# Performance work log

Hardware: AMD Instinct MI355X
Metric: run time of the kernel (lower is better)

The kernel has to match this reference:

```python
import jax, jax.numpy as jnp
import numpy as np

B, N_ATOMS, N_PROBES, N_EDGES = 4, 1250, 50000, 125000
T, D, SH_DIM, NUM_BASIS = 3, 128, 16, 10
CUTOFF = 4.0
NUM_NEIGHBORS = 20.0


def spherical_harmonics_l3(u):
    """Real spherical harmonics l=0..3, component normalization (||Y_l||^2 = 2l+1 on unit vectors). u: [E,3] unit vectors."""
    x, y, z = u[:, 0], u[:, 1], u[:, 2]
    x2, y2, z2 = x * x, y * y, z * z
    s3 = np.sqrt(3.0)
    s15 = np.sqrt(15.0)
    sh = [
        jnp.ones_like(x),                       # l=0
        s3 * x, s3 * y, s3 * z,                 # l=1
        s15 * x * y,                            # l=2
        s15 * y * z,
        (np.sqrt(5.0) / 2.0) * (3.0 * z2 - 1.0),
        s15 * x * z,
        (s15 / 2.0) * (x2 - y2),
        np.sqrt(35.0 / 8.0) * y * (3.0 * x2 - y2),   # l=3
        np.sqrt(105.0) * x * y * z,
        np.sqrt(21.0 / 8.0) * y * (5.0 * z2 - 1.0),
        (np.sqrt(7.0) / 2.0) * (5.0 * z2 * z - 3.0 * z),
        np.sqrt(21.0 / 8.0) * x * (5.0 * z2 - 1.0),
        (np.sqrt(105.0) / 2.0) * z * (x2 - y2),
        np.sqrt(35.0 / 8.0) * x * (x2 - 3.0 * y2),
    ]
    return jnp.stack(sh, axis=-1)  # [E, 16]


def radial_basis(r):
    """Normalized gaussian radial basis on [0, CUTOFF] (e3nn soft_one_hot_linspace style). r: [E]."""
    centers = jnp.linspace(0.0, CUTOFF, NUM_BASIS)
    step = CUTOFF / (NUM_BASIS - 1)
    diff = (r[:, None] - centers) / step
    return jnp.exp(-diff * diff) * 1.12  # [E, NUM_BASIS]


def setup_inputs() -> dict:
    key = jax.random.key(0)
    ks = jax.random.split(key, 10)
    atom_xyz = 6.0 * jax.random.uniform(ks[0], (B, N_ATOMS, 3), jnp.float32)
    probe_xyz = 6.0 * jax.random.uniform(ks[1], (B, N_PROBES, 3), jnp.float32)
    src = jax.random.randint(ks[2], (B, N_EDGES, 1), 0, N_ATOMS)
    dst = jax.random.randint(ks[3], (B, N_EDGES, 1), 0, N_PROBES)
    probe_edges = jnp.concatenate([src, dst], axis=-1).astype(jnp.int32)
    ped = jax.random.randint(ks[4], (B, N_EDGES, 3), -1, 2).astype(jnp.float32)
    cell = jnp.broadcast_to(6.0 * jnp.eye(3, dtype=jnp.float32), (B, 3, 3)) \
        + 0.05 * jax.random.normal(ks[5], (B, 3, 3), jnp.float32)
    atom_rep = jax.random.normal(ks[6], (T, B * N_ATOMS, D), jnp.float32)
    w1 = 0.3 * jax.random.normal(ks[7], (T, NUM_BASIS, 100), jnp.float32)
    w2 = 0.1 * jax.random.normal(ks[8], (T, 100, SH_DIM), jnp.float32)
    w_out = 0.05 * jax.random.normal(ks[9], (D, 1), jnp.float32)
    return {
        "atom_xyz": atom_xyz, "probe_xyz": probe_xyz, "probe_edges": probe_edges,
        "probe_edges_displacement": ped, "cell": cell,
        "num_nodes": jnp.full((B,), N_ATOMS, jnp.int32),
        "num_probes": jnp.full((B,), N_PROBES, jnp.int32),
        "num_probe_edges": jnp.full((B,), N_EDGES, jnp.int32),
        "atom_rep": atom_rep, "w1": w1, "w2": w2, "w_out": w_out,
    }


def reference(atom_xyz, probe_xyz, probe_edges, probe_edges_displacement, cell,
              num_nodes, num_probes, num_probe_edges, atom_rep, w1, w2, w_out):
    b, n = atom_xyz.shape[:2]
    p = probe_xyz.shape[1]
    atoms = atom_xyz.reshape(-1, 3)          # [b*n, 3]  (unpad_and_cat, equal lengths)
    probes_xyz = probe_xyz.reshape(-1, 3)    # [b*p, 3]
    zero = jnp.zeros((1,), num_nodes.dtype)
    node_off = jnp.cumsum(jnp.concatenate([zero, num_nodes[:-1]]))
    probe_off = jnp.cumsum(jnp.concatenate([zero, num_probes[:-1]]))
    off = jnp.stack([node_off, probe_off], axis=-1)[:, None, :]  # [b,1,2]
    edges = (probe_edges + off).reshape(-1, 2)                   # [E,2]
    src, dst = edges[:, 0], edges[:, 1]
    # fractional shift -> cartesian displacement via per-sample cell (repeat_interleave)
    disp = jnp.einsum('bec,bcd->bed', probe_edges_displacement, cell).reshape(-1, 3)
    vec = probes_xyz[dst] - (atoms[src] + disp)                  # [E,3]
    r = jnp.linalg.norm(vec, axis=1)
    u = vec / jnp.maximum(r, 1e-9)[:, None]
    sh = spherical_harmonics_l3(u)                               # [E,16]
    rb = radial_basis(r)                                         # [E,10]
    P = probes_xyz.shape[0]
    probes = jnp.zeros((P, atom_rep.shape[-1]), atom_xyz.dtype)
    inv_sqrt_nn = 1.0 / np.sqrt(NUM_NEIGHBORS)
    for t in range(atom_rep.shape[0]):  # small fixed number of interaction layers
        h = jax.nn.silu(rb @ w1[t]) @ w2[t]          # radial MLP -> per-edge sh weights [E,16]
        scal = jnp.sum(h * sh, axis=-1)              # contract with edge attr [E]
        msg = atom_rep[t][src] * scal[:, None]       # gather + modulate [E,D]
        probes = probes + jax.ops.segment_sum(msg, dst, num_segments=P) * inv_sqrt_nn
    out = (probes @ w_out)[:, 0].reshape(b, p)       # readout 0e scalar, pad_and_stack
    return out, probes
```

## Files before the change

kernel.cpp:

```cpp
#include <hip/hip_runtime.h>
#include <math.h>

#define B_ 4
#define NA 1250
#define NP 50000
#define NE 125000
#define T_ 3
#define D_ 128
#define SHD 16
#define NB 10
#define HID 100
#define E_TOT (B_*NE)
#define P_TOT (B_*NP)
#define A_TOT (B_*NA)
#define INV_SQRT_NN 0.22360679774997896f
#define SCAN_NBLK ((P_TOT + 1023) / 1024)

#define GRID_N 8192
#define RMAX 24.0f
#define FSTR (T_*SHD)

__global__ __launch_bounds__(256) void build_table_kernel(
    const float* __restrict__ w1, const float* __restrict__ w2,
    float* __restrict__ ftab)
{
    int idx = blockIdx.x*256 + threadIdx.x;
    if (idx >= T_*GRID_N) return;
    int t = idx >> 13;
    int ri = idx & (GRID_N-1);

    float r = (float)ri * (RMAX / (float)(GRID_N-1));
    float rb[NB];
    float rs = r * (9.0f / 4.0f);
    #pragma unroll
    for (int i = 0; i < NB; ++i) {
        float dif = rs - (float)i;
        rb[i] = __expf(-dif*dif) * 1.12f;
    }

    float fk[SHD];
    #pragma unroll
    for (int k = 0; k < SHD; ++k) fk[k] = 0.0f;

    for (int j = 0; j < HID; ++j) {
        float h = 0.0f;
        #pragma unroll
        for (int i = 0; i < NB; ++i)
            h += rb[i] * w1[(size_t)(t*NB + i)*HID + j];
        float s = h / (1.0f + __expf(-h));
        #pragma unroll
        for (int k = 0; k < SHD; ++k)
            fk[k] += s * w2[(size_t)(t*HID + j)*SHD + k];
    }

    float* dstp = ftab + (size_t)ri*FSTR + t*SHD;
    #pragma unroll
    for (int k = 0; k < SHD; ++k) dstp[k] = fk[k];
}

__global__ __launch_bounds__(256) void edge_kernel(
    const float* __restrict__ atom_xyz, const float* __restrict__ probe_xyz,
    const int* __restrict__ probe_edges, const float* __restrict__ ped,
    const float* __restrict__ cell, const float* __restrict__ ftab,
    int* __restrict__ counts, int* __restrict__ rank,
    int* __restrict__ dstf, int* __restrict__ srcf, float* __restrict__ scal)
{
    int e = blockIdx.x * 256 + threadIdx.x;
    if (e >= E_TOT) return;
    int b  = e / NE;
    int le = e - b * NE;

    int sl = probe_edges[(size_t)b*NE*2 + (size_t)le*2 + 0];
    int dl = probe_edges[(size_t)b*NE*2 + (size_t)le*2 + 1];
    int src = sl + b * NA;
    int dst = dl + b * NP;

    float p0 = ped[(size_t)b*NE*3 + (size_t)le*3 + 0];
    float p1 = ped[(size_t)b*NE*3 + (size_t)le*3 + 1];
    float p2 = ped[(size_t)b*NE*3 + (size_t)le*3 + 2];
    const float* cb = cell + b*9;
    float dx = p0*cb[0] + p1*cb[3] + p2*cb[6];
    float dy = p0*cb[1] + p1*cb[4] + p2*cb[7];
    float dz = p0*cb[2] + p1*cb[5] + p2*cb[8];

    float vx = probe_xyz[(size_t)dst*3+0] - (atom_xyz[(size_t)src*3+0] + dx);
    float vy = probe_xyz[(size_t)dst*3+1] - (atom_xyz[(size_t)src*3+1] + dy);
    float vz = probe_xyz[(size_t)dst*3+2] - (atom_xyz[(size_t)src*3+2] + dz);
    float r = sqrtf(vx*vx + vy*vy + vz*vz);
    float rinv = 1.0f / fmaxf(r, 1e-9f);
    float x = vx*rinv, y = vy*rinv, z = vz*rinv;
    float x2 = x*x, y2 = y*y, z2 = z*z;

    const float S3  = 1.7320508075688772f;
    const float S15 = 3.872983346207417f;
    float sh[SHD];
    sh[0]  = 1.0f;
    sh[1]  = S3 * x;
    sh[2]  = S3 * y;
    sh[3]  = S3 * z;
    sh[4]  = S15 * x * y;
    sh[5]  = S15 * y * z;
    sh[6]  = 1.118033988749895f * (3.0f*z2 - 1.0f);
    sh[7]  = S15 * x * z;
    sh[8]  = 1.9364916731037085f * (x2 - y2);
    sh[9]  = 2.091650066335189f  * y * (3.0f*x2 - y2);
    sh[10] = 10.246950765959598f * x * y * z;
    sh[11] = 1.6201851746019651f * y * (5.0f*z2 - 1.0f);
    sh[12] = 1.3228756555322954f * (5.0f*z2*z - 3.0f*z);
    sh[13] = 1.6201851746019651f * x * (5.0f*z2 - 1.0f);
    sh[14] = 5.123475382979799f  * z * (x2 - y2);
    sh[15] = 2.091650066335189f  * x * (x2 - 3.0f*y2);

    float u = r * ((float)(GRID_N-1) / RMAX);
    int i0 = (int)u;
    i0 = (i0 > GRID_N-2) ? (GRID_N-2) : i0;
    float w = u - (float)i0;
    const float* F0 = ftab + (size_t)i0 * FSTR;
    const float* F1 = F0 + FSTR;

    #pragma unroll
    for (int t = 0; t < T_; ++t) {
        float d0 = 0.0f, d1 = 0.0f;
        #pragma unroll
        for (int k = 0; k < SHD; ++k) {
            d0 += F0[t*SHD + k] * sh[k];
            d1 += F1[t*SHD + k] * sh[k];
        }
        scal[(size_t)e*3 + t] = d0 + w * (d1 - d0);
    }

    int rk = atomicAdd(&counts[dst], 1);
    rank[e] = rk;
    dstf[e] = dst;
    srcf[e] = src;
}

__global__ __launch_bounds__(256) void scan1_kernel(const int* __restrict__ counts,
                                                    int* __restrict__ starts,
                                                    int* __restrict__ bsums)
{
    __shared__ int sd[256];
    int base = blockIdx.x*1024 + threadIdx.x*4;
    int v0 = (base+0 < P_TOT) ? counts[base+0] : 0;
    int v1 = (base+1 < P_TOT) ? counts[base+1] : 0;
    int v2 = (base+2 < P_TOT) ? counts[base+2] : 0;
    int v3 = (base+3 < P_TOT) ? counts[base+3] : 0;
    int s = v0+v1+v2+v3;
    sd[threadIdx.x] = s;
    __syncthreads();
    for (int off = 1; off < 256; off <<= 1) {
        int t = (threadIdx.x >= off) ? sd[threadIdx.x - off] : 0;
        __syncthreads();
        sd[threadIdx.x] += t;
        __syncthreads();
    }
    int excl = sd[threadIdx.x] - s;
    if (base+0 < P_TOT) starts[base+0] = excl;
    if (base+1 < P_TOT) starts[base+1] = excl + v0;
    if (base+2 < P_TOT) starts[base+2] = excl + v0 + v1;
    if (base+3 < P_TOT) starts[base+3] = excl + v0 + v1 + v2;
    if (threadIdx.x == 255) bsums[blockIdx.x] = sd[255];
}

__global__ __launch_bounds__(256) void scan2_kernel(int* __restrict__ bsums, int n)
{
    __shared__ int sd[256];
    int s = (threadIdx.x < n) ? bsums[threadIdx.x] : 0;
    sd[threadIdx.x] = s;
    __syncthreads();
    for (int off = 1; off < 256; off <<= 1) {
        int t = (threadIdx.x >= off) ? sd[threadIdx.x - off] : 0;
        __syncthreads();
        sd[threadIdx.x] += t;
        __syncthreads();
    }
    if (threadIdx.x < n) bsums[threadIdx.x] = sd[threadIdx.x] - s;
}

__global__ __launch_bounds__(256) void scan3_kernel(int* __restrict__ starts,
                                                    const int* __restrict__ bsums)
{
    int add = bsums[blockIdx.x];
    int base = blockIdx.x*1024 + threadIdx.x*4;
    #pragma unroll
    for (int k = 0; k < 4; ++k)
        if (base+k < P_TOT) starts[base+k] += add;
}

__global__ __launch_bounds__(256) void scatter_kernel(const int* __restrict__ dstf,
                                                      const int* __restrict__ rank,
                                                      const int* __restrict__ starts,
                                                      const int* __restrict__ srcf,
                                                      const float* __restrict__ scal,
                                                      int* __restrict__ srcf_s,
                                                      float* __restrict__ scal_s)
{
    int e = blockIdx.x*256 + threadIdx.x;
    if (e >= E_TOT) return;
    int pos = starts[dstf[e]] + rank[e];
    srcf_s[pos] = srcf[e];
    float s0 = scal[(size_t)e*3+0];
    float s1 = scal[(size_t)e*3+1];
    float s2 = scal[(size_t)e*3+2];
    scal_s[(size_t)pos*3+0] = s0;
    scal_s[(size_t)pos*3+1] = s1;
    scal_s[(size_t)pos*3+2] = s2;
}

__global__ __launch_bounds__(256) void gather_kernel(
    const int* __restrict__ counts, const int* __restrict__ starts,
    const int* __restrict__ srcf_s, const float* __restrict__ scal_s,
    const float* __restrict__ atom_rep, const float* __restrict__ w_out,
    float* __restrict__ out, float* __restrict__ probes)
{
    int wave = threadIdx.x >> 6;
    int lane = threadIdx.x & 63;
    int p = blockIdx.x*4 + wave;

    int st  = starts[p];
    int cnt = counts[p];
    const float2* rep2 = (const float2*)atom_rep;
    const size_t TSTRIDE = (size_t)A_TOT * (D_/2);

    float ax = 0.0f, ay = 0.0f;
    for (int i = 0; i < cnt; ++i) {
        int src = srcf_s[st + i];
        float s0 = scal_s[(size_t)(st+i)*3 + 0];
        float s1 = scal_s[(size_t)(st+i)*3 + 1];
        float s2 = scal_s[(size_t)(st+i)*3 + 2];
        size_t ro = (size_t)src * (D_/2) + lane;
        float2 a0 = rep2[ro];
        float2 a1 = rep2[TSTRIDE + ro];
        float2 a2 = rep2[2*TSTRIDE + ro];
        ax += s0*a0.x + s1*a1.x + s2*a2.x;
        ay += s0*a0.y + s1*a1.y + s2*a2.y;
    }
    ax *= INV_SQRT_NN;
    ay *= INV_SQRT_NN;
    ((float2*)probes)[(size_t)p*(D_/2) + lane] = make_float2(ax, ay);

    float ov = ax*w_out[2*lane] + ay*w_out[2*lane+1];
    #pragma unroll
    for (int off = 32; off > 0; off >>= 1) ov += __shfl_down(ov, off);
    if (lane == 0) out[p] = ov;
}

extern "C" void kernel_launch(void* const* d_in, const int* in_sizes, int n_in,
                              void* d_out, int out_size, void* d_ws, size_t ws_size,
                              hipStream_t stream) {
    const float* atom_xyz  = (const float*)d_in[0];
    const float* probe_xyz = (const float*)d_in[1];
    const int*   probe_edges = (const int*)d_in[2];
    const float* ped       = (const float*)d_in[3];
    const float* cell      = (const float*)d_in[4];
    const float* atom_rep  = (const float*)d_in[8];
    const float* w1        = (const float*)d_in[9];
    const float* w2        = (const float*)d_in[10];
    const float* w_out     = (const float*)d_in[11];

    float* out    = (float*)d_out;
    float* probes = out + P_TOT;

    int* counts     = (int*)d_ws;
    int* starts     = counts + P_TOT;
    int* bsums      = starts + P_TOT;
    int* rank       = bsums + 256;
    int* dstf       = rank + E_TOT;
    int* srcf       = dstf + E_TOT;
    int* srcf_s     = srcf + E_TOT;
    float* scal     = (float*)(srcf_s + E_TOT);
    float* scal_s   = scal + (size_t)E_TOT*3;
    float* ftab     = scal_s + (size_t)E_TOT*3;

    hipMemsetAsync(counts, 0, P_TOT*sizeof(int), stream);

    build_table_kernel<<<(T_*GRID_N + 255)/256, 256, 0, stream>>>(w1, w2, ftab);

    edge_kernel<<<(E_TOT + 255)/256, 256, 0, stream>>>(
        atom_xyz, probe_xyz, probe_edges, ped, cell, ftab,
        counts, rank, dstf, srcf, scal);

    scan1_kernel<<<SCAN_NBLK, 256, 0, stream>>>(counts, starts, bsums);
    scan2_kernel<<<1, 256, 0, stream>>>(bsums, SCAN_NBLK);
    scan3_kernel<<<SCAN_NBLK, 256, 0, stream>>>(starts, bsums);
    scatter_kernel<<<(E_TOT + 255)/256, 256, 0, stream>>>(
        dstf, rank, starts, srcf, scal, srcf_s, scal_s);

    gather_kernel<<<P_TOT/4, 256, 0, stream>>>(
        counts, starts, srcf_s, scal_s, atom_rep, w_out, out, probes);
}
```

Before: 325.0 us.

## Count edges first, then fuse edge compute with CSR scatter into packed float4

A lightweight count pass now builds per-probe counts, the scan runs on them, and the edge kernel computes the scalars and writes them directly into their sorted slot as a packed float4 (three scalars plus the source index). This removes the separate scatter kernel and the intermediate rank, dst, src and scal arrays. The gather kernel reads one float4 per edge, unrolls by 4 so row loads overlap, uses readfirstlane for the segment bounds, and writes probes with nontemporal stores. The cost is a second atomic counter array and an extra pass that reads the edge list.

```diff
diff --git a/kernel.cpp b/kernel.cpp
--- a/kernel.cpp
+++ b/kernel.cpp
@@ -20,6 +20,8 @@
 #define RMAX 24.0f
 #define FSTR (T_*SHD)
 
+typedef float f32x2 __attribute__((ext_vector_type(2)));
+
 __global__ __launch_bounds__(256) void build_table_kernel(
     const float* __restrict__ w1, const float* __restrict__ w2,
     float* __restrict__ ftab)
@@ -58,26 +60,87 @@
     for (int k = 0; k < SHD; ++k) dstp[k] = fk[k];
 }
 
-__global__ __launch_bounds__(256) void edge_kernel(
+__global__ __launch_bounds__(256) void count_kernel(const int* __restrict__ probe_edges,
+                                                    int* __restrict__ counts)
+{
+    int e = blockIdx.x*256 + threadIdx.x;
+    if (e >= E_TOT) return;
+    int b = e / NE;
+    int dl = probe_edges[(size_t)e*2 + 1];
+    atomicAdd(&counts[dl + b*NP], 1);
+}
+
+__global__ __launch_bounds__(256) void scan1_kernel(const int* __restrict__ counts,
+                                                    int* __restrict__ starts,
+                                                    int* __restrict__ bsums)
+{
+    __shared__ int sd[256];
+    int base = blockIdx.x*1024 + threadIdx.x*4;
+    int v0 = (base+0 < P_TOT) ? counts[base+0] : 0;
+    int v1 = (base+1 < P_TOT) ? counts[base+1] : 0;
+    int v2 = (base+2 < P_TOT) ? counts[base+2] : 0;
+    int v3 = (base+3 < P_TOT) ? counts[base+3] : 0;
+    int s = v0+v1+v2+v3;
+    sd[threadIdx.x] = s;
+    __syncthreads();
+    for (int off = 1; off < 256; off <<= 1) {
+        int t = (threadIdx.x >= off) ? sd[threadIdx.x - off] : 0;
+        __syncthreads();
+        sd[threadIdx.x] += t;
+        __syncthreads();
+    }
+    int excl = sd[threadIdx.x] - s;
+    if (base+0 < P_TOT) starts[base+0] = excl;
+    if (base+1 < P_TOT) starts[base+1] = excl + v0;
+    if (base+2 < P_TOT) starts[base+2] = excl + v0 + v1;
+    if (base+3 < P_TOT) starts[base+3] = excl + v0 + v1 + v2;
+    if (threadIdx.x == 255) bsums[blockIdx.x] = sd[255];
+}
+
+__global__ __launch_bounds__(256) void scan2_kernel(int* __restrict__ bsums, int n)
+{
+    __shared__ int sd[256];
+    int s = (threadIdx.x < n) ? bsums[threadIdx.x] : 0;
+    sd[threadIdx.x] = s;
+    __syncthreads();
+    for (int off = 1; off < 256; off <<= 1) {
+        int t = (threadIdx.x >= off) ? sd[threadIdx.x - off] : 0;
+        __syncthreads();
+        sd[threadIdx.x] += t;
+        __syncthreads();
+    }
+    if (threadIdx.x < n) bsums[threadIdx.x] = sd[threadIdx.x] - s;
+}
+
+__global__ __launch_bounds__(256) void scan3_kernel(int* __restrict__ starts,
+                                                    const int* __restrict__ bsums)
+{
+    int add = bsums[blockIdx.x];
+    int base = blockIdx.x*1024 + threadIdx.x*4;
+    #pragma unroll
+    for (int k = 0; k < 4; ++k)
+        if (base+k < P_TOT) starts[base+k] += add;
+}
+
+__global__ __launch_bounds__(256) void edge_scatter_kernel(
     const float* __restrict__ atom_xyz, const float* __restrict__ probe_xyz,
     const int* __restrict__ probe_edges, const float* __restrict__ ped,
     const float* __restrict__ cell, const float* __restrict__ ftab,
-    int* __restrict__ counts, int* __restrict__ rank,
-    int* __restrict__ dstf, int* __restrict__ srcf, float* __restrict__ scal)
+    const int* __restrict__ starts, int* __restrict__ counts2,
+    float4* __restrict__ edge4)
 {
     int e = blockIdx.x * 256 + threadIdx.x;
     if (e >= E_TOT) return;
     int b  = e / NE;
-    int le = e - b * NE;
-
-    int sl = probe_edges[(size_t)b*NE*2 + (size_t)le*2 + 0];
-    int dl = probe_edges[(size_t)b*NE*2 + (size_t)le*2 + 1];
+
+    int sl = probe_edges[(size_t)e*2 + 0];
+    int dl = probe_edges[(size_t)e*2 + 1];
     int src = sl + b * NA;
     int dst = dl + b * NP;
 
-    float p0 = ped[(size_t)b*NE*3 + (size_t)le*3 + 0];
-    float p1 = ped[(size_t)b*NE*3 + (size_t)le*3 + 1];
-    float p2 = ped[(size_t)b*NE*3 + (size_t)le*3 + 2];
+    float p0 = ped[(size_t)e*3 + 0];
+    float p1 = ped[(size_t)e*3 + 1];
+    float p2 = ped[(size_t)e*3 + 2];
     const float* cb = cell + b*9;
     float dx = p0*cb[0] + p1*cb[3] + p2*cb[6];
     float dy = p0*cb[1] + p1*cb[4] + p2*cb[7];
@@ -118,6 +181,7 @@
     const float* F0 = ftab + (size_t)i0 * FSTR;
     const float* F1 = F0 + FSTR;
 
+    float sc[T_];
     #pragma unroll
     for (int t = 0; t < T_; ++t) {
         float d0 = 0.0f, d1 = 0.0f;
@@ -126,118 +190,64 @@
             d0 += F0[t*SHD + k] * sh[k];
             d1 += F1[t*SHD + k] * sh[k];
         }
-        scal[(size_t)e*3 + t] = d0 + w * (d1 - d0);
-    }
-
-    int rk = atomicAdd(&counts[dst], 1);
-    rank[e] = rk;
-    dstf[e] = dst;
-    srcf[e] = src;
-}
-
-__global__ __launch_bounds__(256) void scan1_kernel(const int* __restrict__ counts,
-                                                    int* __restrict__ starts,
-                                                    int* __restrict__ bsums)
-{
-    __shared__ int sd[256];
-    int base = blockIdx.x*1024 + threadIdx.x*4;
-    int v0 = (base+0 < P_TOT) ? counts[base+0] : 0;
-    int v1 = (base+1 < P_TOT) ? counts[base+1] : 0;
-    int v2 = (base+2 < P_TOT) ? counts[base+2] : 0;
-    int v3 = (base+3 < P_TOT) ? counts[base+3] : 0;
-    int s = v0+v1+v2+v3;
-    sd[threadIdx.x] = s;
-    __syncthreads();
-    for (int off = 1; off < 256; off <<= 1) {
-        int t = (threadIdx.x >= off) ? sd[threadIdx.x - off] : 0;
-        __syncthreads();
-        sd[threadIdx.x] += t;
-        __syncthreads();
-    }
-    int excl = sd[threadIdx.x] - s;
-    if (base+0 < P_TOT) starts[base+0] = excl;
-    if (base+1 < P_TOT) starts[base+1] = excl + v0;
-    if (base+2 < P_TOT) starts[base+2] = excl + v0 + v1;
-    if (base+3 < P_TOT) starts[base+3] = excl + v0 + v1 + v2;
-    if (threadIdx.x == 255) bsums[blockIdx.x] = sd[255];
-}
-
-__global__ __launch_bounds__(256) void scan2_kernel(int* __restrict__ bsums, int n)
-{
-    __shared__ int sd[256];
-    int s = (threadIdx.x < n) ? bsums[threadIdx.x] : 0;
-    sd[threadIdx.x] = s;
-    __syncthreads();
-    for (int off = 1; off < 256; off <<= 1) {
-        int t = (threadIdx.x >= off) ? sd[threadIdx.x - off] : 0;
-        __syncthreads();
-        sd[threadIdx.x] += t;
-        __syncthreads();
-    }
-    if (threadIdx.x < n) bsums[threadIdx.x] = sd[threadIdx.x] - s;
-}
-
-__global__ __launch_bounds__(256) void scan3_kernel(int* __restrict__ starts,
-                                                    const int* __restrict__ bsums)
-{
-    int add = bsums[blockIdx.x];
-    int base = blockIdx.x*1024 + threadIdx.x*4;
-    #pragma unroll
-    for (int k = 0; k < 4; ++k)
-        if (base+k < P_TOT) starts[base+k] += add;
-}
-
-__global__ __launch_bounds__(256) void scatter_kernel(const int* __restrict__ dstf,
-                                                      const int* __restrict__ rank,
-                                                      const int* __restrict__ starts,
-                                                      const int* __restrict__ srcf,
-                                                      const float* __restrict__ scal,
-                                                      int* __restrict__ srcf_s,
-                                                      float* __restrict__ scal_s)
-{
-    int e = blockIdx.x*256 + threadIdx.x;
-    if (e >= E_TOT) return;
-    int pos = starts[dstf[e]] + rank[e];
-    srcf_s[pos] = srcf[e];
-    float s0 = scal[(size_t)e*3+0];
-    float s1 = scal[(size_t)e*3+1];
-    float s2 = scal[(size_t)e*3+2];
-    scal_s[(size_t)pos*3+0] = s0;
-    scal_s[(size_t)pos*3+1] = s1;
-    scal_s[(size_t)pos*3+2] = s2;
+        sc[t] = d0 + w * (d1 - d0);
+    }
+
+    int pos = starts[dst] + atomicAdd(&counts2[dst], 1);
+    edge4[pos] = make_float4(sc[0], sc[1], sc[2], __int_as_float(src));
 }
 
 __global__ __launch_bounds__(256) void gather_kernel(
     const int* __restrict__ counts, const int* __restrict__ starts,
-    const int* __restrict__ srcf_s, const float* __restrict__ scal_s,
-    const float* __restrict__ atom_rep, const float* __restrict__ w_out,
+    const float4* __restrict__ edge4, const float* __restrict__ atom_rep,
+    const float* __restrict__ w_out,
     float* __restrict__ out, float* __restrict__ probes)
 {
-    int wave = threadIdx.x >> 6;
     int lane = threadIdx.x & 63;
-    int p = blockIdx.x*4 + wave;
-
-    int st  = starts[p];
-    int cnt = counts[p];
+    int wv   = threadIdx.x >> 6;
+    int p = blockIdx.x*4 + wv;
+
+    int st  = __builtin_amdgcn_readfirstlane(starts[p]);
+    int cnt = __builtin_amdgcn_readfirstlane(counts[p]);
+
     const float2* rep2 = (const float2*)atom_rep;
-    const size_t TSTRIDE = (size_t)A_TOT * (D_/2);
+    const size_t TS = (size_t)A_TOT * (D_/2);
 
     float ax = 0.0f, ay = 0.0f;
-    for (int i = 0; i < cnt; ++i) {
-        int src = srcf_s[st + i];
-        float s0 = scal_s[(size_t)(st+i)*3 + 0];
-        float s1 = scal_s[(size_t)(st+i)*3 + 1];
-        float s2 = scal_s[(size_t)(st+i)*3 + 2];
-        size_t ro = (size_t)src * (D_/2) + lane;
-        float2 a0 = rep2[ro];
-        float2 a1 = rep2[TSTRIDE + ro];
-        float2 a2 = rep2[2*TSTRIDE + ro];
-        ax += s0*a0.x + s1*a1.x + s2*a2.x;
-        ay += s0*a0.y + s1*a1.y + s2*a2.y;
-    }
+
+    for (int base = 0; base < cnt; base += 4) {
+        int m = cnt - base;
+        float4 e0, e1, e2, e3;
+        e0 = edge4[st+base];
+        if (m > 1) e1 = edge4[st+base+1];
+        if (m > 2) e2 = edge4[st+base+2];
+        if (m > 3) e3 = edge4[st+base+3];
+
+        float2 a00,a01,a02, a10,a11,a12, a20,a21,a22, a30,a31,a32;
+        {           size_t ro = (size_t)__float_as_int(e0.w)*(D_/2) + lane;
+                    a00 = rep2[ro]; a01 = rep2[TS+ro]; a02 = rep2[2*TS+ro]; }
+        if (m > 1) { size_t ro = (size_t)__float_as_int(e1.w)*(D_/2) + lane;
+                    a10 = rep2[ro]; a11 = rep2[TS+ro]; a12 = rep2[2*TS+ro]; }
+        if (m > 2) { size_t ro = (size_t)__float_as_int(e2.w)*(D_/2) + lane;
+                    a20 = rep2[ro]; a21 = rep2[TS+ro]; a22 = rep2[2*TS+ro]; }
+        if (m > 3) { size_t ro = (size_t)__float_as_int(e3.w)*(D_/2) + lane;
+                    a30 = rep2[ro]; a31 = rep2[TS+ro]; a32 = rep2[2*TS+ro]; }
+
+        ax += e0.x*a00.x + e0.y*a01.x + e0.z*a02.x;
+        ay += e0.x*a00.y + e0.y*a01.y + e0.z*a02.y;
+        if (m > 1) { ax += e1.x*a10.x + e1.y*a11.x + e1.z*a12.x;
+                     ay += e1.x*a10.y + e1.y*a11.y + e1.z*a12.y; }
+        if (m > 2) { ax += e2.x*a20.x + e2.y*a21.x + e2.z*a22.x;
+                     ay += e2.x*a20.y + e2.y*a21.y + e2.z*a22.y; }
+        if (m > 3) { ax += e3.x*a30.x + e3.y*a31.x + e3.z*a32.x;
+                     ay += e3.x*a30.y + e3.y*a31.y + e3.z*a32.y; }
+    }
+
     ax *= INV_SQRT_NN;
     ay *= INV_SQRT_NN;
-    ((float2*)probes)[(size_t)p*(D_/2) + lane] = make_float2(ax, ay);
+
+    f32x2 v; v.x = ax; v.y = ay;
+    __builtin_nontemporal_store(v, (f32x2*)(probes) + (size_t)p*(D_/2) + lane);
 
     float ov = ax*w_out[2*lane] + ay*w_out[2*lane+1];
     #pragma unroll
@@ -261,31 +271,27 @@
     float* out    = (float*)d_out;
     float* probes = out + P_TOT;
 
-    int* counts     = (int*)d_ws;
-    int* starts     = counts + P_TOT;
-    int* bsums      = starts + P_TOT;
-    int* rank       = bsums + 256;
-    int* dstf       = rank + E_TOT;
-    int* srcf       = dstf + E_TOT;
-    int* srcf_s     = srcf + E_TOT;
-    float* scal     = (float*)(srcf_s + E_TOT);
-    float* scal_s   = scal + (size_t)E_TOT*3;
-    float* ftab     = scal_s + (size_t)E_TOT*3;
-
-    hipMemsetAsync(counts, 0, P_TOT*sizeof(int), stream);
+    float4* edge4 = (float4*)d_ws;
+    float*  ftab  = (float*)(edge4 + E_TOT);
+    int* counts   = (int*)(ftab + (size_t)GRID_N*FSTR);
+    int* counts2  = counts + P_TOT;
+    int* starts   = counts2 + P_TOT;
+    int* bsums    = starts + P_TOT;
+
+    hipMemsetAsync(counts, 0, 2*P_TOT*sizeof(int), stream);
 
     build_table_kernel<<<(T_*GRID_N + 255)/256, 256, 0, stream>>>(w1, w2, ftab);
 
-    edge_kernel<<<(E_TOT + 255)/256, 256, 0, stream>>>(
-        atom_xyz, probe_xyz, probe_edges, ped, cell, ftab,
-        counts, rank, dstf, srcf, scal);
+    count_kernel<<<(E_TOT + 255)/256, 256, 0, stream>>>(probe_edges, counts);
 
     scan1_kernel<<<SCAN_NBLK, 256, 0, stream>>>(counts, starts, bsums);
     scan2_kernel<<<1, 256, 0, stream>>>(bsums, SCAN_NBLK);
     scan3_kernel<<<SCAN_NBLK, 256, 0, stream>>>(starts, bsums);
-    scatter_kernel<<<(E_TOT + 255)/256, 256, 0, stream>>>(
-        dstf, rank, starts, srcf, scal, srcf_s, scal_s);
+
+    edge_scatter_kernel<<<(E_TOT + 255)/256, 256, 0, stream>>>(
+        atom_xyz, probe_xyz, probe_edges, ped, cell, ftab,
+        starts, counts2, edge4);
 
     gather_kernel<<<P_TOT/4, 256, 0, stream>>>(
-        counts, starts, srcf_s, scal_s, atom_rep, w_out, out, probes);
-}
+        counts, starts, edge4, atom_rep, w_out, out, probes);
+}
```

New measurement: 306.1 us. -5.8%, faster.
